# Kernel optimization log

Measured on AMD Instinct MI355X. Metric: run time of the kernel, lower is better.

## Reference

```python
import jax, jax.numpy as jnp
import numpy as np

B, N = 64, 1024


def setup_inputs() -> dict:
    key = jax.random.key(0)
    k1, k2, k3, k4 = jax.random.split(key, 4)
    successor_logits = jax.random.normal(k1, (B, N, N), dtype=jnp.float32)
    predecessor_logits = jax.random.normal(k2, (B, N, N), dtype=jnp.float32)
    # labels in [-1, N); -1 means 'points to self'
    successor_labels = jax.random.randint(k3, (B, N), -1, N, dtype=jnp.int64)
    predecessor_labels = jax.random.randint(k4, (B, N), -1, N, dtype=jnp.int64)
    line_mask = jnp.ones((B, N), dtype=bool)
    return {
        "successor_logits": successor_logits,
        "successor_labels": successor_labels,
        "predecessor_logits": predecessor_logits,
        "predecessor_labels": predecessor_labels,
        "line_mask": line_mask,
        "pred_weight": jnp.float32(1.0),
    }


def _direction_loss(logits, labels, line_mask, is_self_pointing):
    b, n = labels.shape
    line_idx = jnp.arange(n)
    # relabel self-pointing lines to their own index
    labels_fixed = jnp.where(is_self_pointing, line_idx[None, :], labels)
    # overwrite diagonal logit with (row max + 1) where self-pointing & valid
    row_max = jnp.max(logits, axis=-1)  # [B, N]
    cond = is_self_pointing & line_mask  # [B, N]
    eye = jnp.eye(n, dtype=bool)
    logits_adj = jnp.where(cond[:, :, None] & eye[None], (row_max + 1.0)[:, :, None], logits)
    # softmax cross-entropy per line
    logp = jax.nn.log_softmax(logits_adj, axis=-1)  # [B, N, N]
    lbl = jnp.clip(labels_fixed, 0, n - 1)
    nll = -jnp.take_along_axis(logp, lbl[:, :, None], axis=-1)[..., 0]  # [B, N]
    valid = line_mask.astype(logits.dtype)
    denom = jnp.maximum(valid.sum(), 1.0)
    return (nll * valid).sum() / denom


def reference(successor_logits, successor_labels, predecessor_logits,
              predecessor_labels, line_mask, pred_weight):
    last_line_mask = successor_labels == -1
    succ_loss = _direction_loss(successor_logits, successor_labels, line_mask, last_line_mask)
    first_line_mask = predecessor_labels == -1
    pred_loss = _direction_loss(predecessor_logits, predecessor_labels, line_mask, first_line_mask)
    total_loss = succ_loss + pred_weight * pred_loss
    num_valid = line_mask.sum()
    return total_loss, succ_loss, pred_loss, num_valid
```

## Files before the change

kernel.cpp:

```cpp
#include <hip/hip_runtime.h>
#include <math.h>

#define N_ 1024
#define ROWS_PER_DIR 65536
#define TOTAL_ROWS   131072
#define WAVES_PER_BLOCK 8
#define BLOCKS_K1    (TOTAL_ROWS / WAVES_PER_BLOCK)
#define BLOCKS_PER_DIR (BLOCKS_K1 / 2)

typedef float v4f __attribute__((ext_vector_type(4)));
typedef float v2f __attribute__((ext_vector_type(2)));

__global__ __launch_bounds__(512) void row_loss_kernel(
    const float* __restrict__ succ_logits,
    const int*   __restrict__ succ_labels,
    const float* __restrict__ pred_logits,
    const int*   __restrict__ pred_labels,
    const int*   __restrict__ line_mask,
    v2f*         __restrict__ partials)
{
    __shared__ float wsum[WAVES_PER_BLOCK];
    __shared__ float wcnt[WAVES_PER_BLOCK];
    const int wave = threadIdx.x >> 6;
    const int lane = threadIdx.x & 63;
    const int r    = blockIdx.x * WAVES_PER_BLOCK + wave;
    const int dir  = r >> 16;
    const int rr   = r & (ROWS_PER_DIR - 1);
    const int n    = rr & (N_ - 1);

    const float* __restrict__ logits = dir ? pred_logits : succ_logits;
    const int*   __restrict__ labels = dir ? pred_labels : succ_labels;
    const float* __restrict__ row    = logits + (size_t)rr * N_;

    const int label = labels[rr];
    const int valid = line_mask[rr];

    const v4f* row4 = (const v4f*)row;
    v4f v0 = __builtin_nontemporal_load(row4 + 0 * 64 + lane);
    v4f v1 = __builtin_nontemporal_load(row4 + 1 * 64 + lane);
    v4f v2 = __builtin_nontemporal_load(row4 + 2 * 64 + lane);
    v4f v3 = __builtin_nontemporal_load(row4 + 3 * 64 + lane);

    const int t      = (label == -1) ? n : (label < 0 ? 0 : (label > N_ - 1 ? N_ - 1 : label));
    const int t_lane = (t >> 2) & 63;
    const int t_k    = t >> 8;
    const int t_c    = t & 3;
    v4f tv = (t_k == 0) ? v0 : (t_k == 1) ? v1 : (t_k == 2) ? v2 : v3;
    const float x_t = __shfl(tv[t_c], t_lane);

    float m;
    {
        v4f a = v0, b = v1;
        a.x = fmaxf(a.x, b.x); a.y = fmaxf(a.y, b.y); a.z = fmaxf(a.z, b.z); a.w = fmaxf(a.w, b.w);
        v4f c = v2; b = v3;
        c.x = fmaxf(c.x, b.x); c.y = fmaxf(c.y, b.y); c.z = fmaxf(c.z, b.z); c.w = fmaxf(c.w, b.w);
        a.x = fmaxf(a.x, c.x); a.y = fmaxf(a.y, c.y); a.z = fmaxf(a.z, c.z); a.w = fmaxf(a.w, c.w);
        m = fmaxf(fmaxf(a.x, a.y), fmaxf(a.z, a.w));
    }
    #pragma unroll
    for (int off = 32; off > 0; off >>= 1)
        m = fmaxf(m, __shfl_xor(m, off));

    float s = 0.0f;
    s += __expf(v0.x - m); s += __expf(v0.y - m); s += __expf(v0.z - m); s += __expf(v0.w - m);
    s += __expf(v1.x - m); s += __expf(v1.y - m); s += __expf(v1.z - m); s += __expf(v1.w - m);
    s += __expf(v2.x - m); s += __expf(v2.y - m); s += __expf(v2.z - m); s += __expf(v2.w - m);
    s += __expf(v3.x - m); s += __expf(v3.y - m); s += __expf(v3.z - m); s += __expf(v3.w - m);
    #pragma unroll
    for (int off = 32; off > 0; off >>= 1)
        s += __shfl_xor(s, off);

    if (lane == 0) {
        float nll = 0.0f;
        if (valid) {
            if (label == -1) {
                nll = __logf((s - __expf(x_t - m)) * 0.36787944117144233f + 1.0f);
            } else {
                nll = m + __logf(s) - x_t;
            }
        }
        wsum[wave] = nll;
        wcnt[wave] = (dir == 0 && valid) ? 1.0f : 0.0f;
    }
    __syncthreads();
    if (threadIdx.x == 0) {
        float acc = 0.0f, cnt = 0.0f;
        #pragma unroll
        for (int w = 0; w < WAVES_PER_BLOCK; ++w) { acc += wsum[w]; cnt += wcnt[w]; }
        v2f p; p.x = acc; p.y = cnt;
        partials[blockIdx.x] = p;
    }
}

__global__ __launch_bounds__(1024) void finalize_kernel(
    const v2f*   __restrict__ partials,
    const float* __restrict__ pred_weight,
    float*       __restrict__ out)
{
    const int tid = threadIdx.x;
    float ssum = 0.0f, psum = 0.0f, msum = 0.0f;
    for (int i = tid; i < BLOCKS_PER_DIR; i += 1024) {
        v2f sp = partials[i];
        v2f pp = partials[i + BLOCKS_PER_DIR];
        ssum += sp.x;
        msum += sp.y;
        psum += pp.x;
    }

    #pragma unroll
    for (int off = 32; off > 0; off >>= 1) {
        ssum += __shfl_xor(ssum, off);
        psum += __shfl_xor(psum, off);
        msum += __shfl_xor(msum, off);
    }

    __shared__ float sh[3][16];
    const int wave = tid >> 6, lane = tid & 63;
    if (lane == 0) { sh[0][wave] = ssum; sh[1][wave] = psum; sh[2][wave] = msum; }
    __syncthreads();
    if (tid == 0) {
        float S = 0.0f, P = 0.0f, M = 0.0f;
        #pragma unroll
        for (int w = 0; w < 16; ++w) { S += sh[0][w]; P += sh[1][w]; M += sh[2][w]; }
        const float denom = fmaxf(M, 1.0f);
        const float sl = S / denom, pl = P / denom;
        const float w  = pred_weight[0];
        out[0] = sl + w * pl;
        out[1] = sl;
        out[2] = pl;
        out[3] = M;
    }
}

extern "C" void kernel_launch(void* const* d_in, const int* in_sizes, int n_in,
                              void* d_out, int out_size, void* d_ws, size_t ws_size,
                              hipStream_t stream) {
    const float* succ_logits = (const float*)d_in[0];
    const int*   succ_labels = (const int*)  d_in[1];
    const float* pred_logits = (const float*)d_in[2];
    const int*   pred_labels = (const int*)  d_in[3];
    const int*   line_mask   = (const int*)  d_in[4];
    const float* pred_weight = (const float*)d_in[5];
    float* out      = (float*)d_out;
    v2f*   partials = (v2f*)d_ws;

    row_loss_kernel<<<BLOCKS_K1, 512, 0, stream>>>(
        succ_logits, succ_labels, pred_logits, pred_labels, line_mask, partials);
    finalize_kernel<<<1, 1024, 0, stream>>>(partials, pred_weight, out);
}
```

Before: 477.1 us.

## Process multiple rows per wave with register double-buffered prefetch

Each wave now handles eight consecutive rows instead of one. It prefetches the next row's logits into a second register set while it computes the current row's softmax cross-entropy. Labels and masks are loaded once per wave and broadcast with shuffles, and the block-level shared-memory reduction and __syncthreads are removed in favour of one partial per wave. The aim is to cut launch, block scheduling and barrier overhead and to overlap memory loads with computation. The cost is more registers per thread and fewer waves in flight across the GPU.

Result: no change. 484.1 us (+1.4%).

```diff
diff --git a/kernel.cpp b/kernel.cpp
--- a/kernel.cpp
+++ b/kernel.cpp
@@ -4,9 +4,11 @@
 #define N_ 1024
 #define ROWS_PER_DIR 65536
 #define TOTAL_ROWS   131072
+#define ROWS_PER_WAVE 8
 #define WAVES_PER_BLOCK 8
-#define BLOCKS_K1    (TOTAL_ROWS / WAVES_PER_BLOCK)
-#define BLOCKS_PER_DIR (BLOCKS_K1 / 2)
+#define VBLOCKS      (TOTAL_ROWS / ROWS_PER_WAVE)
+#define BLOCKS_K1    (VBLOCKS / WAVES_PER_BLOCK)
+#define BLOCKS_PER_DIR (VBLOCKS / 2)
 
 typedef float v4f __attribute__((ext_vector_type(4)));
 typedef float v2f __attribute__((ext_vector_type(2)));
@@ -19,58 +21,75 @@
     const int*   __restrict__ line_mask,
     v2f*         __restrict__ partials)
 {
-    __shared__ float wsum[WAVES_PER_BLOCK];
-    __shared__ float wcnt[WAVES_PER_BLOCK];
     const int wave = threadIdx.x >> 6;
     const int lane = threadIdx.x & 63;
-    const int r    = blockIdx.x * WAVES_PER_BLOCK + wave;
-    const int dir  = r >> 16;
-    const int rr   = r & (ROWS_PER_DIR - 1);
-    const int n    = rr & (N_ - 1);
+    const int vb   = blockIdx.x * WAVES_PER_BLOCK + wave;
+    const int r0   = vb * ROWS_PER_WAVE;
+    const int dir  = r0 >> 16;
+    const int rr0  = r0 & (ROWS_PER_DIR - 1);
 
     const float* __restrict__ logits = dir ? pred_logits : succ_logits;
     const int*   __restrict__ labels = dir ? pred_labels : succ_labels;
-    const float* __restrict__ row    = logits + (size_t)rr * N_;
 
-    const int label = labels[rr];
-    const int valid = line_mask[rr];
+    int lbl = 0, msk = 0;
+    if (lane < ROWS_PER_WAVE) {
+        lbl = labels[rr0 + lane];
+        msk = line_mask[rr0 + lane];
+    }
 
-    const v4f* row4 = (const v4f*)row;
-    v4f v0 = __builtin_nontemporal_load(row4 + 0 * 64 + lane);
-    v4f v1 = __builtin_nontemporal_load(row4 + 1 * 64 + lane);
-    v4f v2 = __builtin_nontemporal_load(row4 + 2 * 64 + lane);
-    v4f v3 = __builtin_nontemporal_load(row4 + 3 * 64 + lane);
+    const v4f* __restrict__ base4 = (const v4f*)(logits + (size_t)rr0 * N_);
 
-    const int t      = (label == -1) ? n : (label < 0 ? 0 : (label > N_ - 1 ? N_ - 1 : label));
-    const int t_lane = (t >> 2) & 63;
-    const int t_k    = t >> 8;
-    const int t_c    = t & 3;
-    v4f tv = (t_k == 0) ? v0 : (t_k == 1) ? v1 : (t_k == 2) ? v2 : v3;
-    const float x_t = __shfl(tv[t_c], t_lane);
+    v4f a0 = __builtin_nontemporal_load(base4 + 0 * 64 + lane);
+    v4f a1 = __builtin_nontemporal_load(base4 + 1 * 64 + lane);
+    v4f a2 = __builtin_nontemporal_load(base4 + 2 * 64 + lane);
+    v4f a3 = __builtin_nontemporal_load(base4 + 3 * 64 + lane);
 
-    float m;
-    {
-        v4f a = v0, b = v1;
-        a.x = fmaxf(a.x, b.x); a.y = fmaxf(a.y, b.y); a.z = fmaxf(a.z, b.z); a.w = fmaxf(a.w, b.w);
-        v4f c = v2; b = v3;
-        c.x = fmaxf(c.x, b.x); c.y = fmaxf(c.y, b.y); c.z = fmaxf(c.z, b.z); c.w = fmaxf(c.w, b.w);
-        a.x = fmaxf(a.x, c.x); a.y = fmaxf(a.y, c.y); a.z = fmaxf(a.z, c.z); a.w = fmaxf(a.w, c.w);
-        m = fmaxf(fmaxf(a.x, a.y), fmaxf(a.z, a.w));
-    }
+    float acc = 0.0f, cnt = 0.0f;
+
     #pragma unroll
-    for (int off = 32; off > 0; off >>= 1)
-        m = fmaxf(m, __shfl_xor(m, off));
+    for (int k = 0; k < ROWS_PER_WAVE; ++k) {
+        v4f b0, b1, b2, b3;
+        if (k < ROWS_PER_WAVE - 1) {
+            const v4f* nb = base4 + (size_t)(k + 1) * 256;
+            b0 = __builtin_nontemporal_load(nb + 0 * 64 + lane);
+            b1 = __builtin_nontemporal_load(nb + 1 * 64 + lane);
+            b2 = __builtin_nontemporal_load(nb + 2 * 64 + lane);
+            b3 = __builtin_nontemporal_load(nb + 3 * 64 + lane);
+        }
 
-    float s = 0.0f;
-    s += __expf(v0.x - m); s += __expf(v0.y - m); s += __expf(v0.z - m); s += __expf(v0.w - m);
-    s += __expf(v1.x - m); s += __expf(v1.y - m); s += __expf(v1.z - m); s += __expf(v1.w - m);
-    s += __expf(v2.x - m); s += __expf(v2.y - m); s += __expf(v2.z - m); s += __expf(v2.w - m);
-    s += __expf(v3.x - m); s += __expf(v3.y - m); s += __expf(v3.z - m); s += __expf(v3.w - m);
-    #pragma unroll
-    for (int off = 32; off > 0; off >>= 1)
-        s += __shfl_xor(s, off);
+        const int label = __shfl(lbl, k);
+        const int valid = __shfl(msk, k);
+        const int n     = (rr0 + k) & (N_ - 1);
 
-    if (lane == 0) {
+        const int t      = (label == -1) ? n : (label < 0 ? 0 : (label > N_ - 1 ? N_ - 1 : label));
+        const int t_lane = (t >> 2) & 63;
+        const int t_k    = t >> 8;
+        const int t_c    = t & 3;
+        v4f tv = (t_k == 0) ? a0 : (t_k == 1) ? a1 : (t_k == 2) ? a2 : a3;
+        const float x_t = __shfl(tv[t_c], t_lane);
+
+        float m;
+        {
+            v4f a = a0, b = a1;
+            a.x = fmaxf(a.x, b.x); a.y = fmaxf(a.y, b.y); a.z = fmaxf(a.z, b.z); a.w = fmaxf(a.w, b.w);
+            v4f c = a2; b = a3;
+            c.x = fmaxf(c.x, b.x); c.y = fmaxf(c.y, b.y); c.z = fmaxf(c.z, b.z); c.w = fmaxf(c.w, b.w);
+            a.x = fmaxf(a.x, c.x); a.y = fmaxf(a.y, c.y); a.z = fmaxf(a.z, c.z); a.w = fmaxf(a.w, c.w);
+            m = fmaxf(fmaxf(a.x, a.y), fmaxf(a.z, a.w));
+        }
+        #pragma unroll
+        for (int off = 32; off > 0; off >>= 1)
+            m = fmaxf(m, __shfl_xor(m, off));
+
+        float s = 0.0f;
+        s += __expf(a0.x - m); s += __expf(a0.y - m); s += __expf(a0.z - m); s += __expf(a0.w - m);
+        s += __expf(a1.x - m); s += __expf(a1.y - m); s += __expf(a1.z - m); s += __expf(a1.w - m);
+        s += __expf(a2.x - m); s += __expf(a2.y - m); s += __expf(a2.z - m); s += __expf(a2.w - m);
+        s += __expf(a3.x - m); s += __expf(a3.y - m); s += __expf(a3.z - m); s += __expf(a3.w - m);
+        #pragma unroll
+        for (int off = 32; off > 0; off >>= 1)
+            s += __shfl_xor(s, off);
+
         float nll = 0.0f;
         if (valid) {
             if (label == -1) {
@@ -79,16 +98,15 @@
                 nll = m + __logf(s) - x_t;
             }
         }
-        wsum[wave] = nll;
-        wcnt[wave] = (dir == 0 && valid) ? 1.0f : 0.0f;
+        acc += nll;
+        cnt += (dir == 0 && valid) ? 1.0f : 0.0f;
+
+        if (k < ROWS_PER_WAVE - 1) { a0 = b0; a1 = b1; a2 = b2; a3 = b3; }
     }
-    __syncthreads();
-    if (threadIdx.x == 0) {
-        float acc = 0.0f, cnt = 0.0f;
-        #pragma unroll
-        for (int w = 0; w < WAVES_PER_BLOCK; ++w) { acc += wsum[w]; cnt += wcnt[w]; }
+
+    if (lane == 0) {
         v2f p; p.x = acc; p.y = cnt;
-        partials[blockIdx.x] = p;
+        partials[vb] = p;
     }
 }
 
```
